# Kernel tuning notes

Measured on AMD Instinct MI355X. Metric: run time of the kernel, lower is better.

## Reference

```python
import jax, jax.numpy as jnp
import numpy as np

# ---- module hyperparameters (init_kwargs) ----
H, W = 200, 200
V = H * W
WIN = 7
BETA = 0.5
CELL_X, CELL_Y = 0.5, 0.5
DIST_SCALE = 2.0
EPS = 0.1
N_ITERS = 30
N_LIST = (1, 2, 3, 4, 5)
B, T = 32, 64


def _precompute_buffers():
    """Neighbor ids/validity for all V cells + distance-decayed kernel weights."""
    r = WIN // 2
    dy, dx = np.meshgrid(np.arange(-r, r + 1), np.arange(-r, r + 1), indexing='ij')
    offsets = np.stack([dy, dx], -1).reshape(-1, 2)          # (K,2)
    dist_km = np.hypot(dy * CELL_Y, dx * CELL_X).reshape(-1) * DIST_SCALE
    kernel_w = np.exp(-BETA * dist_km).astype(np.float32)    # (K,)
    ids = np.arange(V)
    rr, cc = ids // W, ids % W
    rn = rr[:, None] + offsets[None, :, 0]
    cn = cc[:, None] + offsets[None, :, 1]
    valid = (rn >= 0) & (rn < H) & (cn >= 0) & (cn < W)      # (V,K)
    nb = np.clip(rn, 0, H - 1) * W + np.clip(cn, 0, W - 1)   # (V,K)
    return kernel_w, nb.astype(np.int32), valid


def setup_inputs() -> dict:
    key = jax.random.key(0)
    k1, k2 = jax.random.split(key)
    kernel_w, nb_ids_all, valid_all = _precompute_buffers()
    return {
        'logits': jax.random.normal(k1, (B, T, V), dtype=jnp.float32),
        'target_ids': jax.random.randint(k2, (B, T), 0, V),
        'kernel_w': jnp.asarray(kernel_w),
        'nb_ids_all': jnp.asarray(nb_ids_all),
        'valid_all': jnp.asarray(valid_all),
        'weights': jnp.full((len(N_LIST),), 1.0 / len(N_LIST), dtype=jnp.float32),
    }


def _unigram_U(p, target_ids, kernel_w, nb_ids_all, valid_all):
    """U[b,i,j] = sum_k p[b,i, nb[target[b,j],k]] * w[b,j,k], w normalized over k."""
    nb = nb_ids_all[target_ids]                      # (B,T,K) int
    valid = valid_all[target_ids]                    # (B,T,K) bool
    w = valid.astype(p.dtype) * kernel_w[None, None, :].astype(p.dtype)
    w = w / jnp.clip(w.sum(-1, keepdims=True), 1e-12)

    def per_batch(P, nb_b, w_b):                     # P:(T,V) nb_b:(T,K) w_b:(T,K)
        vals = P[:, nb_b]                            # (T,T,K): vals[i,j,k] = P[i, nb_b[j,k]]
        return jnp.einsum('ijk,jk->ij', vals, w_b)   # (T,T)

    U = jax.vmap(per_batch)(p, nb, w)                # (B,T,T)
    return jnp.clip(U, 1e-12)


def _ngram_S(U, n):
    """S[b,i,j] = prod_{k<n} U[b,i+k,j+k]; via shifted-window products (no strides)."""
    I = U.shape[1] - n + 1
    S = U[:, :I, :I]
    for k in range(1, n):
        S = S * U[:, k:I + k, k:I + k]
    return jnp.clip(S, 1e-12)


def _sinkhorn(S):
    Bn, I, J = S.shape
    mu = jnp.full((Bn, I), 1.0 / I, dtype=S.dtype)
    nu = jnp.full((Bn, J), 1.0 / J, dtype=S.dtype)
    K = jnp.clip(jnp.exp(S / EPS), 1e-30)

    def step(carry, _):
        a, b = carry
        a = mu / jnp.clip(jnp.einsum('bij,bj->bi', K, b), 1e-30)
        b = nu / jnp.clip(jnp.einsum('bij,bi->bj', K, a), 1e-30)
        return (a, b), None

    (a, b), _ = jax.lax.scan(step, (jnp.ones_like(mu), jnp.ones_like(nu)), None, length=N_ITERS)
    return a[:, :, None] * K * b[:, None, :]


def reference(logits, target_ids, kernel_w, nb_ids_all, valid_all, weights):
    p = jax.nn.softmax(logits, axis=-1)
    U = _unigram_U(p, target_ids, kernel_w, nb_ids_all, valid_all)
    per_sample = jnp.zeros(U.shape[0], dtype=U.dtype)
    for i, n in enumerate(N_LIST):
        S = _ngram_S(U, n)
        M = _sinkhorn(S)
        q_n = jnp.clip((M * S).sum(axis=(-1, -2)), 1e-12)
        per_sample = per_sample - weights[i] * jnp.log(q_n)
    return per_sample.mean()
```

## Files before the change

### kernel.cpp

```cpp
#include <hip/hip_runtime.h>
#include <hip/hip_bf16.h>

#define H_    200
#define W_    200
#define V_    40000
#define WIN_  7
#define K49   49
#define B_    32
#define T_    64
#define NLIST 5
#define NITER 30

__global__ void k_prep(const int* __restrict__ target,
                       const float* __restrict__ kernel_w,
                       int* __restrict__ idx_tab,
                       float* __restrict__ w_tab)
{
    int bj = blockIdx.x * blockDim.x + threadIdx.x;
    if (bj >= B_ * T_) return;
    int t  = target[bj];
    int rr = t / W_, cc = t % W_;

    float ssum = 0.f;
    for (int k = 0; k < K49; ++k) {
        int dy = k / 7 - 3, dx = k % 7 - 3;
        int rn = rr + dy, cn = cc + dx;
        bool val = (rn >= 0) && (rn < H_) && (cn >= 0) && (cn < W_);
        if (val) ssum += kernel_w[k];
    }
    float den = fmaxf(ssum, 1e-12f);
    for (int k = 0; k < K49; ++k) {
        int dy = k / 7 - 3, dx = k % 7 - 3;
        int rn = rr + dy, cn = cc + dx;
        bool val = (rn >= 0) && (rn < H_) && (cn >= 0) && (cn < W_);
        int rc  = min(max(rn, 0), H_ - 1);
        int ccl = min(max(cn, 0), W_ - 1);
        idx_tab[bj * K49 + k] = rc * W_ + ccl;
        w_tab[bj * K49 + k]   = val ? (kernel_w[k] / den) : 0.f;
    }
}

__global__ __launch_bounds__(256) void k_softmax_u(
    const float* __restrict__ logits,
    const int* __restrict__ idx_tab,
    const float* __restrict__ w_tab,
    float* __restrict__ U)
{
    int bi = blockIdx.x;
    int b  = bi >> 6;
    const float* row = logits + (size_t)bi * V_;

    __shared__ int   sIdx[T_ * K49];
    __shared__ float sW  [T_ * K49];
    __shared__ float red[4];

    for (int t = threadIdx.x; t < T_ * K49; t += 256) {
        sIdx[t] = idx_tab[b * T_ * K49 + t];
        sW[t]   = w_tab  [b * T_ * K49 + t];
    }

    float s = 0.f;
    const float4* row4 = (const float4*)row;
    for (int v = threadIdx.x; v < V_ / 4; v += 256) {
        float4 x = row4[v];
        s += __expf(x.x) + __expf(x.y) + __expf(x.z) + __expf(x.w);
    }
#pragma unroll
    for (int off = 32; off > 0; off >>= 1) s += __shfl_xor(s, off);
    if ((threadIdx.x & 63) == 0) red[threadIdx.x >> 6] = s;
    __syncthreads();
    float inv_denom = 1.f / (red[0] + red[1] + red[2] + red[3]);

    int j = threadIdx.x >> 2, part = threadIdx.x & 3;
    float acc = 0.f;
    for (int k = part; k < K49; k += 4) {
        int id = sIdx[j * K49 + k];
        acc += __expf(row[id]) * sW[j * K49 + k];
    }
    acc += __shfl_xor(acc, 1);
    acc += __shfl_xor(acc, 2);
    if (part == 0)
        U[(size_t)bi * T_ + j] = fmaxf(acc * inv_denom, 1e-12f);
}

__global__ __launch_bounds__(256) void k_sinkhorn(
    const float* __restrict__ U, float* __restrict__ qout)
{
    int b = blockIdx.x / NLIST;
    int n = blockIdx.x % NLIST + 1;
    int I = T_ - n + 1;
    const int LD = 65;

    __shared__ float Ssh[64 * 65];
    __shared__ float Ksh[64 * 65];
    __shared__ float av[64], bv[64];
    __shared__ float red[4];

    const float* Ub = U + (size_t)b * T_ * T_;

    for (int idx = threadIdx.x; idx < I * I; idx += 256) {
        int i = idx / I;
        int j = idx - i * I;
        float p = Ub[i * T_ + j];
        for (int k = 1; k < n; ++k) p *= Ub[(i + k) * T_ + (j + k)];
        p = fmaxf(p, 1e-12f);
        Ssh[i * LD + j] = p;
        Ksh[i * LD + j] = __expf(p * 10.0f);
    }
    if (threadIdx.x < 64) bv[threadIdx.x] = 1.0f;
    __syncthreads();

    float mu = 1.0f / (float)I;
    int i4 = threadIdx.x >> 2, part = threadIdx.x & 3;

    for (int it = 0; it < NITER; ++it) {
        if (i4 < I) {
            float r = 0.f;
            for (int j = part; j < I; j += 4) r += Ksh[i4 * LD + j] * bv[j];
            r += __shfl_xor(r, 1);
            r += __shfl_xor(r, 2);
            if (part == 0) av[i4] = mu / fmaxf(r, 1e-30f);
        }
        __syncthreads();
        if (i4 < I) {
            float r = 0.f;
            for (int i = part; i < I; i += 4) r += Ksh[i * LD + i4] * av[i];
            r += __shfl_xor(r, 1);
            r += __shfl_xor(r, 2);
            if (part == 0) bv[i4] = mu / fmaxf(r, 1e-30f);
        }
        __syncthreads();
    }

    float q = 0.f;
    for (int idx = threadIdx.x; idx < I * I; idx += 256) {
        int i = idx / I;
        int j = idx - i * I;
        q += av[i] * Ksh[i * LD + j] * bv[j] * Ssh[i * LD + j];
    }
#pragma unroll
    for (int off = 32; off > 0; off >>= 1) q += __shfl_xor(q, off);
    if ((threadIdx.x & 63) == 0) red[threadIdx.x >> 6] = q;
    __syncthreads();
    if (threadIdx.x == 0)
        qout[blockIdx.x] = fmaxf(red[0] + red[1] + red[2] + red[3], 1e-12f);
}

__global__ void k_final(const float* __restrict__ qout,
                        const float* __restrict__ weights,
                        float* __restrict__ out)
{
    __shared__ float red[4];
    float s = 0.f;
    int t = threadIdx.x;
    if (t < B_ * NLIST) {
        int n = t % NLIST;
        s = -weights[n] * logf(qout[t]);
    }
#pragma unroll
    for (int off = 32; off > 0; off >>= 1) s += __shfl_xor(s, off);
    if ((t & 63) == 0) red[t >> 6] = s;
    __syncthreads();
    if (t == 0) out[0] = (red[0] + red[1] + red[2] + red[3]) / (float)B_;
}

extern "C" void kernel_launch(void* const* d_in, const int* in_sizes, int n_in,
                              void* d_out, int out_size, void* d_ws, size_t ws_size,
                              hipStream_t stream)
{
    const float* logits   = (const float*)d_in[0];
    const int*   target   = (const int*)  d_in[1];
    const float* kernel_w = (const float*)d_in[2];
    const float* weights  = (const float*)d_in[5];
    float* out = (float*)d_out;

    float* w_tab   = (float*)d_ws;
    int*   idx_tab = (int*)(w_tab + B_ * T_ * K49);
    float* Ubuf    = (float*)(idx_tab + B_ * T_ * K49);
    float* qbuf    = Ubuf + B_ * T_ * T_;

    k_prep<<<(B_ * T_ + 255) / 256, 256, 0, stream>>>(target, kernel_w, idx_tab, w_tab);
    k_softmax_u<<<B_ * T_, 256, 0, stream>>>(logits, idx_tab, w_tab, Ubuf);
    k_sinkhorn<<<B_ * NLIST, 256, 0, stream>>>(Ubuf, qbuf);
    k_final<<<1, 256, 0, stream>>>(qbuf, weights, out);
}
```

Measured before the change: 561.8 us.

## Fuse prep into softmax kernel and rewrite Sinkhorn as single-wave register kernel

Neighbor index and weight computation moves into the softmax/U kernel, which drops the prep launch and its shared-memory staging. The final reduction is replaced by atomicAdd into an output that the softmax kernel zeroes. Sinkhorn becomes one 64-lane wave per (batch, n). K rows and columns are held in registers, vectors are broadcast with readlane instead of shared memory and barriers, and n is a template parameter. The costs are heavy register pressure (128+ floats per lane), only 160 single-wave blocks, and nondeterministic atomic summation.

Result: faster. 480.1 us (-14.6%).

```diff
diff --git a/kernel.cpp b/kernel.cpp
--- a/kernel.cpp
+++ b/kernel.cpp
@@ -4,164 +4,180 @@
 #define H_    200
 #define W_    200
 #define V_    40000
-#define WIN_  7
 #define K49   49
 #define B_    32
 #define T_    64
-#define NLIST 5
 #define NITER 30
 
-__global__ void k_prep(const int* __restrict__ target,
-                       const float* __restrict__ kernel_w,
-                       int* __restrict__ idx_tab,
-                       float* __restrict__ w_tab)
-{
-    int bj = blockIdx.x * blockDim.x + threadIdx.x;
-    if (bj >= B_ * T_) return;
-    int t  = target[bj];
-    int rr = t / W_, cc = t % W_;
-
-    float ssum = 0.f;
-    for (int k = 0; k < K49; ++k) {
-        int dy = k / 7 - 3, dx = k % 7 - 3;
-        int rn = rr + dy, cn = cc + dx;
-        bool val = (rn >= 0) && (rn < H_) && (cn >= 0) && (cn < W_);
-        if (val) ssum += kernel_w[k];
-    }
-    float den = fmaxf(ssum, 1e-12f);
-    for (int k = 0; k < K49; ++k) {
-        int dy = k / 7 - 3, dx = k % 7 - 3;
-        int rn = rr + dy, cn = cc + dx;
-        bool val = (rn >= 0) && (rn < H_) && (cn >= 0) && (cn < W_);
-        int rc  = min(max(rn, 0), H_ - 1);
-        int ccl = min(max(cn, 0), W_ - 1);
-        idx_tab[bj * K49 + k] = rc * W_ + ccl;
-        w_tab[bj * K49 + k]   = val ? (kernel_w[k] / den) : 0.f;
-    }
+__device__ __forceinline__ float rl(float v, int l) {
+    return __int_as_float(__builtin_amdgcn_readlane(__float_as_int(v), l));
 }
 
 __global__ __launch_bounds__(256) void k_softmax_u(
     const float* __restrict__ logits,
-    const int* __restrict__ idx_tab,
-    const float* __restrict__ w_tab,
-    float* __restrict__ U)
+    const int* __restrict__ target,
+    const float* __restrict__ kernel_w,
+    float* __restrict__ U,
+    float* __restrict__ out_zero)
 {
     int bi = blockIdx.x;
     int b  = bi >> 6;
+    if (bi == 0 && threadIdx.x == 0) out_zero[0] = 0.f;
     const float* row = logits + (size_t)bi * V_;
-
-    __shared__ int   sIdx[T_ * K49];
-    __shared__ float sW  [T_ * K49];
     __shared__ float red[4];
 
-    for (int t = threadIdx.x; t < T_ * K49; t += 256) {
-        sIdx[t] = idx_tab[b * T_ * K49 + t];
-        sW[t]   = w_tab  [b * T_ * K49 + t];
+    int j = threadIdx.x >> 2, part = threadIdx.x & 3;
+    int tgt = target[b * T_ + j];
+    int rr = tgt / W_, cc = tgt - rr * W_;
+
+    int   myIdx[13];
+    float myW[13];
+    float ssum = 0.f;
+#pragma unroll
+    for (int kk = 0; kk < 13; ++kk) {
+        int k  = part + 4 * kk;
+        int kc = (k < K49) ? k : 0;
+        int q7 = kc / 7;
+        int dy = q7 - 3;
+        int dx = (kc - q7 * 7) - 3;
+        int rn = rr + dy, cn = cc + dx;
+        bool val = (k < K49) && (rn >= 0) && (rn < H_) && (cn >= 0) && (cn < W_);
+        int rcl = min(max(rn, 0), H_ - 1);
+        int ccl = min(max(cn, 0), W_ - 1);
+        myIdx[kk] = rcl * W_ + ccl;
+        float w = val ? kernel_w[kc] : 0.f;
+        myW[kk] = w;
+        ssum += w;
     }
+    ssum += __shfl_xor(ssum, 1);
+    ssum += __shfl_xor(ssum, 2);
+    float inv_s = 1.f / fmaxf(ssum, 1e-12f);
 
-    float s = 0.f;
+    float s0 = 0.f, s1 = 0.f;
     const float4* row4 = (const float4*)row;
     for (int v = threadIdx.x; v < V_ / 4; v += 256) {
         float4 x = row4[v];
-        s += __expf(x.x) + __expf(x.y) + __expf(x.z) + __expf(x.w);
+        s0 += __expf(x.x) + __expf(x.y);
+        s1 += __expf(x.z) + __expf(x.w);
     }
+    float s = s0 + s1;
 #pragma unroll
     for (int off = 32; off > 0; off >>= 1) s += __shfl_xor(s, off);
     if ((threadIdx.x & 63) == 0) red[threadIdx.x >> 6] = s;
     __syncthreads();
     float inv_denom = 1.f / (red[0] + red[1] + red[2] + red[3]);
 
-    int j = threadIdx.x >> 2, part = threadIdx.x & 3;
     float acc = 0.f;
-    for (int k = part; k < K49; k += 4) {
-        int id = sIdx[j * K49 + k];
-        acc += __expf(row[id]) * sW[j * K49 + k];
-    }
+#pragma unroll
+    for (int kk = 0; kk < 13; ++kk)
+        acc += __expf(row[myIdx[kk]]) * myW[kk];
     acc += __shfl_xor(acc, 1);
     acc += __shfl_xor(acc, 2);
     if (part == 0)
-        U[(size_t)bi * T_ + j] = fmaxf(acc * inv_denom, 1e-12f);
+        U[(size_t)bi * T_ + j] = fmaxf(acc * inv_s * inv_denom, 1e-12f);
 }
 
-__global__ __launch_bounds__(256) void k_sinkhorn(
-    const float* __restrict__ U, float* __restrict__ qout)
+template<int N>
+__device__ __forceinline__ void sinkhorn_impl(
+    int b, const float* __restrict__ U,
+    const float* __restrict__ weights, float* __restrict__ out)
 {
-    int b = blockIdx.x / NLIST;
-    int n = blockIdx.x % NLIST + 1;
-    int I = T_ - n + 1;
-    const int LD = 65;
+    const int I = T_ - N + 1;
+    int lane = threadIdx.x;
+    __shared__ float Ush[64 * 65];
 
-    __shared__ float Ssh[64 * 65];
-    __shared__ float Ksh[64 * 65];
-    __shared__ float av[64], bv[64];
-    __shared__ float red[4];
-
-    const float* Ub = U + (size_t)b * T_ * T_;
-
-    for (int idx = threadIdx.x; idx < I * I; idx += 256) {
-        int i = idx / I;
-        int j = idx - i * I;
-        float p = Ub[i * T_ + j];
-        for (int k = 1; k < n; ++k) p *= Ub[(i + k) * T_ + (j + k)];
-        p = fmaxf(p, 1e-12f);
-        Ssh[i * LD + j] = p;
-        Ksh[i * LD + j] = __expf(p * 10.0f);
+    const float4* U4 = (const float4*)(U + (size_t)b * T_ * T_);
+#pragma unroll
+    for (int it = 0; it < 16; ++it) {
+        int f = lane + 64 * it;
+        float4 x = U4[f];
+        int r = f >> 4, c = (f & 15) << 2;
+        float* p = &Ush[r * 65 + c];
+        p[0] = x.x; p[1] = x.y; p[2] = x.z; p[3] = x.w;
     }
-    if (threadIdx.x < 64) bv[threadIdx.x] = 1.0f;
     __syncthreads();
 
-    float mu = 1.0f / (float)I;
-    int i4 = threadIdx.x >> 2, part = threadIdx.x & 3;
-
-    for (int it = 0; it < NITER; ++it) {
-        if (i4 < I) {
-            float r = 0.f;
-            for (int j = part; j < I; j += 4) r += Ksh[i4 * LD + j] * bv[j];
-            r += __shfl_xor(r, 1);
-            r += __shfl_xor(r, 2);
-            if (part == 0) av[i4] = mu / fmaxf(r, 1e-30f);
-        }
-        __syncthreads();
-        if (i4 < I) {
-            float r = 0.f;
-            for (int i = part; i < I; i += 4) r += Ksh[i * LD + i4] * av[i];
-            r += __shfl_xor(r, 1);
-            r += __shfl_xor(r, 2);
-            if (part == 0) bv[i4] = mu / fmaxf(r, 1e-30f);
-        }
-        __syncthreads();
+    float Krow[64], Kcol[64];
+#pragma unroll
+    for (int j = 0; j < 64; ++j) {
+        float p = 1.f;
+#pragma unroll
+        for (int k = 0; k < N; ++k)
+            p *= Ush[min(lane + k, 63) * 65 + min(j + k, 63)];
+        p = fmaxf(p, 1e-12f);
+        bool ok = (lane < I) && (j < I);
+        Krow[j] = ok ? __expf(10.f * p) : 0.f;
+    }
+#pragma unroll
+    for (int i = 0; i < 64; ++i) {
+        float p = 1.f;
+#pragma unroll
+        for (int k = 0; k < N; ++k)
+            p *= Ush[min(i + k, 63) * 65 + min(lane + k, 63)];
+        p = fmaxf(p, 1e-12f);
+        bool ok = (i < I) && (lane < I);
+        Kcol[i] = ok ? __expf(10.f * p) : 0.f;
     }
 
-    float q = 0.f;
-    for (int idx = threadIdx.x; idx < I * I; idx += 256) {
-        int i = idx / I;
-        int j = idx - i * I;
-        q += av[i] * Ksh[i * LD + j] * bv[j] * Ssh[i * LD + j];
+    const float mu = 1.f / (float)I;
+    float bj = (lane < I) ? 1.f : 0.f;
+    float ai = 0.f;
+    for (int it = 0; it < NITER; ++it) {
+        float r0 = 0.f, r1 = 0.f, r2 = 0.f, r3 = 0.f;
+#pragma unroll
+        for (int j = 0; j < 64; j += 4) {
+            r0 += Krow[j + 0] * rl(bj, j + 0);
+            r1 += Krow[j + 1] * rl(bj, j + 1);
+            r2 += Krow[j + 2] * rl(bj, j + 2);
+            r3 += Krow[j + 3] * rl(bj, j + 3);
+        }
+        float r = (r0 + r1) + (r2 + r3);
+        ai = (lane < I) ? mu / fmaxf(r, 1e-30f) : 0.f;
+        r0 = r1 = r2 = r3 = 0.f;
+#pragma unroll
+        for (int i = 0; i < 64; i += 4) {
+            r0 += Kcol[i + 0] * rl(ai, i + 0);
+            r1 += Kcol[i + 1] * rl(ai, i + 1);
+            r2 += Kcol[i + 2] * rl(ai, i + 2);
+            r3 += Kcol[i + 3] * rl(ai, i + 3);
+        }
+        r = (r0 + r1) + (r2 + r3);
+        bj = (lane < I) ? mu / fmaxf(r, 1e-30f) : 0.f;
     }
+
+    float rq = 0.f;
 #pragma unroll
-    for (int off = 32; off > 0; off >>= 1) q += __shfl_xor(q, off);
-    if ((threadIdx.x & 63) == 0) red[threadIdx.x >> 6] = q;
-    __syncthreads();
-    if (threadIdx.x == 0)
-        qout[blockIdx.x] = fmaxf(red[0] + red[1] + red[2] + red[3], 1e-12f);
+    for (int j = 0; j < 64; ++j) {
+        float p = 1.f;
+#pragma unroll
+        for (int k = 0; k < N; ++k)
+            p *= Ush[min(lane + k, 63) * 65 + min(j + k, 63)];
+        p = fmaxf(p, 1e-12f);
+        rq += Krow[j] * p * rl(bj, j);
+    }
+    rq *= ai;
+#pragma unroll
+    for (int off = 32; off > 0; off >>= 1) rq += __shfl_xor(rq, off);
+    if (lane == 0) {
+        float q = fmaxf(rq, 1e-12f);
+        atomicAdd(out, -(weights[N - 1] * (1.f / (float)B_)) * __logf(q));
+    }
 }
 
-__global__ void k_final(const float* __restrict__ qout,
-                        const float* __restrict__ weights,
-                        float* __restrict__ out)
+__global__ __launch_bounds__(64) void k_sinkhorn(
+    const float* __restrict__ U,
+    const float* __restrict__ weights,
+    float* __restrict__ out)
 {
-    __shared__ float red[4];
-    float s = 0.f;
-    int t = threadIdx.x;
-    if (t < B_ * NLIST) {
-        int n = t % NLIST;
-        s = -weights[n] * logf(qout[t]);
+    int b = blockIdx.x / 5;
+    int n = blockIdx.x - b * 5;
+    switch (n) {
+    case 0: sinkhorn_impl<1>(b, U, weights, out); break;
+    case 1: sinkhorn_impl<2>(b, U, weights, out); break;
+    case 2: sinkhorn_impl<3>(b, U, weights, out); break;
+    case 3: sinkhorn_impl<4>(b, U, weights, out); break;
+    case 4: sinkhorn_impl<5>(b, U, weights, out); break;
     }
-#pragma unroll
-    for (int off = 32; off > 0; off >>= 1) s += __shfl_xor(s, off);
-    if ((t & 63) == 0) red[t >> 6] = s;
-    __syncthreads();
-    if (t == 0) out[0] = (red[0] + red[1] + red[2] + red[3]) / (float)B_;
 }
 
 extern "C" void kernel_launch(void* const* d_in, const int* in_sizes, int n_in,
@@ -172,15 +188,9 @@
     const int*   target   = (const int*)  d_in[1];
     const float* kernel_w = (const float*)d_in[2];
     const float* weights  = (const float*)d_in[5];
-    float* out = (float*)d_out;
+    float* out  = (float*)d_out;
+    float* Ubuf = (float*)d_ws;
 
-    float* w_tab   = (float*)d_ws;
-    int*   idx_tab = (int*)(w_tab + B_ * T_ * K49);
-    float* Ubuf    = (float*)(idx_tab + B_ * T_ * K49);
-    float* qbuf    = Ubuf + B_ * T_ * T_;
-
-    k_prep<<<(B_ * T_ + 255) / 256, 256, 0, stream>>>(target, kernel_w, idx_tab, w_tab);
-    k_softmax_u<<<B_ * T_, 256, 0, stream>>>(logits, idx_tab, w_tab, Ubuf);
-    k_sinkhorn<<<B_ * NLIST, 256, 0, stream>>>(Ubuf, qbuf);
-    k_final<<<1, 256, 0, stream>>>(qbuf, weights, out);
+    k_softmax_u<<<B_ * T_, 256, 0, stream>>>(logits, target, kernel_w, Ubuf, out);
+    k_sinkhorn<<<B_ * 5, 64, 0, stream>>>(Ubuf, weights, out);
 }
```
